# Performance work log

Measured on AMD Instinct MI355X. Metric: run time of the kernel, lower is better.

## Reference

```python
import jax, jax.numpy as jnp
import numpy as np

B, H, W, C = 8, 128, 128, 256
WS, SS, NH = 8, 4, 8          # window size, shift size, num heads
HD = C // NH                   # head dim = 32
N = WS * WS                    # tokens per window = 64
NW = (H // WS) * (W // WS)     # windows per image = 256


def _rel_pos_index():
    coords = np.stack(np.meshgrid(np.arange(WS), np.arange(WS), indexing='ij'))  # (2,WS,WS)
    cf = coords.reshape(2, -1)
    rc = (cf[:, :, None] - cf[:, None, :]).transpose(1, 2, 0)
    rc[:, :, 0] += WS - 1
    rc[:, :, 1] += WS - 1
    rc[:, :, 0] *= 2 * WS - 1
    return rc.sum(-1)  # (N, N) int


def _attn_mask():
    # shift mask for SW-MSA, built from static shapes (matches torch img_mask construction)
    img = np.zeros((1, H, W, 1))
    sl = (slice(0, -WS), slice(-WS, -SS), slice(-SS, None))
    cnt = 0
    for h in sl:
        for w in sl:
            img[:, h, w, :] = cnt
            cnt += 1
    mw = img.reshape(1, H // WS, WS, W // WS, WS, 1).transpose(0, 1, 3, 2, 4, 5).reshape(-1, N)
    am = mw[:, None, :] - mw[:, :, None]  # (NW, N, N)
    return np.where(am != 0, -100.0, 0.0).astype(np.float32)


RPI = jnp.asarray(_rel_pos_index())      # (N, N)
AMASK = jnp.asarray(_attn_mask())        # (NW, N, N)


def _ln(x, g, b):
    m = x.mean(-1, keepdims=True)
    v = x.var(-1, keepdims=True)
    return (x - m) / jnp.sqrt(v + 1e-5) * g + b


def setup_inputs() -> dict:
    key = jax.random.key(0)
    ks = jax.random.split(key, 8)
    s = lambda k, shp, sc: jax.random.normal(k, shp, jnp.float32) * sc
    return {
        'x': s(ks[0], (B, H * W, C), 1.0),
        'norm1_g': jnp.ones((C,), jnp.float32), 'norm1_b': jnp.zeros((C,), jnp.float32),
        'qkv_w': s(ks[1], (3 * C, C), 0.02), 'qkv_b': jnp.zeros((3 * C,), jnp.float32),
        'rpb_table': s(ks[2], ((2 * WS - 1) ** 2, NH), 0.02),
        'proj_w': s(ks[3], (C, C), 0.02), 'proj_b': jnp.zeros((C,), jnp.float32),
        'norm2_g': jnp.ones((C,), jnp.float32), 'norm2_b': jnp.zeros((C,), jnp.float32),
        'fc1_w': s(ks[4], (4 * C, C), 0.02), 'fc1_b': jnp.zeros((4 * C,), jnp.float32),
        'fc2_w': s(ks[5], (C, 4 * C), 0.02), 'fc2_b': jnp.zeros((C,), jnp.float32),
    }


def reference(x, norm1_g, norm1_b, qkv_w, qkv_b, rpb_table, proj_w, proj_b,
              norm2_g, norm2_b, fc1_w, fc1_b, fc2_w, fc2_b):
    shortcut = x
    h = _ln(x, norm1_g, norm1_b).reshape(B, H, W, C)
    # cyclic shift
    h = jnp.roll(h, (-SS, -SS), axis=(1, 2))
    # window partition -> (B*NW, N, C)
    xw = h.reshape(B, H // WS, WS, W // WS, WS, C).transpose(0, 1, 3, 2, 4, 5).reshape(-1, N, C)
    qkv = (xw @ qkv_w.T + qkv_b).reshape(-1, N, 3, NH, HD).transpose(2, 0, 3, 1, 4)
    q, k, v = qkv[0], qkv[1], qkv[2]           # (B*NW, NH, N, HD)
    attn = jnp.einsum('bhnd,bhmd->bhnm', q * (float(HD) ** -0.5), k)
    bias = rpb_table[RPI.reshape(-1)].reshape(N, N, NH).transpose(2, 0, 1)  # (NH, N, N)
    attn = attn + bias[None]
    attn = attn.reshape(B, NW, NH, N, N) + AMASK[None, :, None]
    attn = jax.nn.softmax(attn.reshape(-1, NH, N, N), axis=-1)
    xw = jnp.einsum('bhnm,bhmd->bnhd', attn, v).reshape(-1, N, C)
    xw = xw @ proj_w.T + proj_b
    # window reverse + reverse shift
    h = xw.reshape(B, H // WS, W // WS, WS, WS, C).transpose(0, 1, 3, 2, 4, 5).reshape(B, H, W, C)
    h = jnp.roll(h, (SS, SS), axis=(1, 2)).reshape(B, H * W, C)
    x = shortcut + h
    # MLP block
    m = _ln(x, norm2_g, norm2_b)
    m = jax.nn.gelu(m @ fc1_w.T + fc1_b, approximate=False) @ fc2_w.T + fc2_b
    return x + m
```

## Files before the change

kernel.cpp:

```cpp
#include <hip/hip_runtime.h>
#include <hip/hip_bf16.h>
#include <math.h>

#define B_   8
#define H_   128
#define W_   128
#define C_   256
#define WS_  8
#define SS_  4
#define NH_  8
#define HD_  32
#define MROWS 131072

typedef short bf16x8 __attribute__((ext_vector_type(8)));
typedef float f32x4  __attribute__((ext_vector_type(4)));

__device__ __forceinline__ unsigned short f2bf(float f) {
    unsigned int u = __float_as_uint(f);
    u += 0x7fffu + ((u >> 16) & 1u);
    return (unsigned short)(u >> 16);
}
__device__ __forceinline__ float bfl(unsigned int u) {
    return __uint_as_float(u << 16);
}
__device__ __forceinline__ float bfh(unsigned int u) {
    return __uint_as_float(u & 0xffff0000u);
}

__device__ __forceinline__ unsigned int pk2(float a, float b) {
    __hip_bfloat162 h = __float22bfloat162_rn(make_float2(a, b));
    unsigned int u;
    __builtin_memcpy(&u, &h, 4);
    return u;
}

__device__ __forceinline__ void gload16(const unsigned short* g, unsigned short* l) {
    __builtin_amdgcn_global_load_lds(
        (const __attribute__((address_space(1))) unsigned int*)(const void*)g,
        (__attribute__((address_space(3))) unsigned int*)(void*)l, 16, 0, 0);
}

__device__ __forceinline__ float fast_gelu2(float v) {
    return v * __builtin_amdgcn_rcpf(1.0f + __expf(-1.702f * v));
}

__global__ __launch_bounds__(256) void cvt4(const float* __restrict__ s,
                                            unsigned short* __restrict__ d, int n) {
    const int i = (blockIdx.x * 256 + threadIdx.x) * 4;
    if (i >= n) return;
    const float4 v = *(const float4*)(s + i);
    ushort4 o;
    o.x = f2bf(v.x); o.y = f2bf(v.y); o.z = f2bf(v.z); o.w = f2bf(v.w);
    *(ushort4*)(d + i) = o;
}

template<int SHIFT>
__global__ __launch_bounds__(256) void ln_kernel(const float* __restrict__ in,
                                                 const float* __restrict__ g,
                                                 const float* __restrict__ b,
                                                 unsigned short* __restrict__ out) {
    const int wid  = threadIdx.x >> 6;
    const int lane = threadIdx.x & 63;
    const int row  = blockIdx.x * 4 + wid;

    int src;
    if (SHIFT) {
        const int bimg = row >> 14;
        const int rem  = row & 16383;
        const int win  = rem >> 6;
        const int tok  = rem & 63;
        const int hp = (win >> 4) * 8 + (tok >> 3);
        const int wp = (win & 15) * 8 + (tok & 7);
        const int ho = (hp + SS_) & (H_ - 1);
        const int wo = (wp + SS_) & (W_ - 1);
        src = (bimg << 14) + ho * W_ + wo;
    } else {
        src = row;
    }

    const float4 v = ((const float4*)(in + (size_t)src * C_))[lane];
    float s  = v.x + v.y + v.z + v.w;
    float ss = v.x*v.x + v.y*v.y + v.z*v.z + v.w*v.w;
#pragma unroll
    for (int o = 1; o < 64; o <<= 1) {
        s  += __shfl_xor(s,  o, 64);
        ss += __shfl_xor(ss, o, 64);
    }
    const float mean = s * (1.0f / C_);
    const float var  = ss * (1.0f / C_) - mean * mean;
    const float rstd = rsqrtf(var + 1e-5f);

    const float4 gg = ((const float4*)g)[lane];
    const float4 bb = ((const float4*)b)[lane];
    ushort4 o4;
    o4.x = f2bf((v.x - mean) * rstd * gg.x + bb.x);
    o4.y = f2bf((v.y - mean) * rstd * gg.y + bb.y);
    o4.z = f2bf((v.z - mean) * rstd * gg.z + bb.z);
    o4.w = f2bf((v.w - mean) * rstd * gg.w + bb.w);
    *(ushort4*)(out + (size_t)row * C_ + lane * 4) = o4;
}

template<int N>
__global__ __launch_bounds__(256, 2) void gemm_nloop(const unsigned short* __restrict__ A,
                                                     const unsigned short* __restrict__ W,
                                                     const float* __restrict__ bias,
                                                     unsigned short* __restrict__ Cout) {
    __shared__ unsigned short W_lds[2][64 * 256];

    const int t    = threadIdx.x;
    const int wave = t >> 6, lane = t & 63;
    const int fr   = lane & 15, h = lane >> 4;
    const int m0   = blockIdx.x * 128;
    constexpr int NT = N / 64;

    bf16x8 aw[2][8];
    const unsigned short* Abase = A + (size_t)(m0 + wave * 32 + fr) * 256 + h * 8;
#pragma unroll
    for (int mi = 0; mi < 2; ++mi)
#pragma unroll
        for (int ks = 0; ks < 8; ++ks)
            aw[mi][ks] = *(const bf16x8*)(Abase + mi * 16 * 256 + ks * 32);

    auto stage = [&](int b, int nt) {
        const unsigned short* Wt = W + (size_t)nt * 64 * 256;
#pragma unroll
        for (int q = 0; q < 8; ++q) {
            const int d    = q * 4096 + t * 16;
            const int row  = d >> 9;
            const int colb = (d & 511) ^ ((row & 7) << 4);
            gload16(Wt + (size_t)row * 256 + (colb >> 1),
                    &W_lds[b][(q * 4096 + wave * 1024) >> 1]);
        }
    };

    stage(0, 0);
    __syncthreads();

    for (int nt = 0; nt < NT; ++nt) {
        if (nt + 1 < NT) stage((nt + 1) & 1, nt + 1);

        const char* buf = (const char*)W_lds[nt & 1];
        f32x4 acc[2][4] = {};
#pragma unroll
        for (int nj = 0; nj < 4; ++nj) {
            const int   wrow = nj * 16 + fr;
            const char* wb   = buf + wrow * 512;
            const int   swz  = (fr & 7) << 4;
            bf16x8 wf[8];
#pragma unroll
            for (int ks = 0; ks < 8; ++ks)
                wf[ks] = *(const bf16x8*)(wb + ((ks * 64 + h * 16) ^ swz));
#pragma unroll
            for (int ks = 0; ks < 8; ++ks) {
                acc[0][nj] = __builtin_amdgcn_mfma_f32_16x16x32_bf16(wf[ks], aw[0][ks], acc[0][nj], 0, 0, 0);
                acc[1][nj] = __builtin_amdgcn_mfma_f32_16x16x32_bf16(wf[ks], aw[1][ks], acc[1][nj], 0, 0, 0);
            }
        }

#pragma unroll
        for (int nj = 0; nj < 4; ++nj) {
            const int n = nt * 64 + nj * 16 + h * 4;
            const float4 bb = *(const float4*)&bias[n];
#pragma unroll
            for (int mi = 0; mi < 2; ++mi) {
                const int m = m0 + wave * 32 + mi * 16 + fr;
                uint2 pk;
                pk.x = pk2(acc[mi][nj][0] + bb.x, acc[mi][nj][1] + bb.y);
                pk.y = pk2(acc[mi][nj][2] + bb.z, acc[mi][nj][3] + bb.w);
                *(uint2*)&Cout[(size_t)m * N + n] = pk;
            }
        }
        __syncthreads();
    }
}

__global__ __launch_bounds__(512, 2) void mlp_fused(const unsigned short* __restrict__ A,
                                                    const unsigned short* __restrict__ W1,
                                                    const float* __restrict__ b1,
                                                    const unsigned short* __restrict__ W2,
                                                    const float* __restrict__ b2,
                                                    const unsigned short* __restrict__ x1b,
                                                    float* __restrict__ out) {
    __shared__ unsigned short W1_lds[2][32 * 256];
    __shared__ unsigned short W2_lds[2][256 * 32];
    __shared__ unsigned short G_lds [256 * 32];

    const int t    = threadIdx.x;
    const int wave = t >> 6, lane = t & 63;
    const int fr   = lane & 15, h = lane >> 4;
    const int wr   = wave >> 2, wc = wave & 3;
    const int m0   = blockIdx.x * 256;
    constexpr int NC = 32;

    bf16x8 aw[2][8];
    const unsigned short* Abase = A + (size_t)(m0 + wave * 32 + fr) * 256 + h * 8;
#pragma unroll
    for (int mi = 0; mi < 2; ++mi)
#pragma unroll
        for (int ks = 0; ks < 8; ++ks)
            aw[mi][ks] = *(const bf16x8*)(Abase + mi * 16 * 256 + ks * 32);

    auto stageW1 = [&](int b, int c) {
        const unsigned short* Wt = W1 + (size_t)c * 32 * 256;
#pragma unroll
        for (int q = 0; q < 2; ++q) {
            const int d    = q * 8192 + t * 16;
            const int row  = d >> 9;
            const int colb = (d & 511) ^ ((row & 7) << 4);
            gload16(Wt + (size_t)row * 256 + (colb >> 1),
                    &W1_lds[b][(q * 8192 + wave * 1024) >> 1]);
        }
    };
    auto stageW2 = [&](int b, int c) {
#pragma unroll
        for (int q = 0; q < 2; ++q) {
            const int d    = q * 8192 + t * 16;
            const int row  = d >> 6;
            const int colb = (d & 63) ^ ((row & 3) << 4);
            gload16(W2 + (size_t)row * 1024 + c * 32 + (colb >> 1),
                    &W2_lds[b][(q * 8192 + wave * 1024) >> 1]);
        }
    };

    auto fc1 = [&](int cc) {
        const char* buf = (const char*)W1_lds[cc & 1];
        const int   swz = (fr & 7) << 4;
#pragma unroll
        for (int nj = 0; nj < 2; ++nj) {
            const int   wrow = nj * 16 + fr;
            const char* wb   = buf + wrow * 512;
            bf16x8 wf[8];
#pragma unroll
            for (int ks = 0; ks < 8; ++ks)
                wf[ks] = *(const bf16x8*)(wb + ((ks * 64 + h * 16) ^ swz));
            f32x4 g0 = {}, g1 = {};
#pragma unroll
            for (int ks = 0; ks < 8; ++ks) {
                g0 = __builtin_amdgcn_mfma_f32_16x16x32_bf16(wf[ks], aw[0][ks], g0, 0, 0, 0);
                g1 = __builtin_amdgcn_mfma_f32_16x16x32_bf16(wf[ks], aw[1][ks], g1, 0, 0, 0);
            }
            const float4 bb = *(const float4*)&b1[cc * 32 + nj * 16 + h * 4];
            {
                const int row = wave * 32 + fr;
                const int off = (nj * 32 + h * 8) ^ ((row & 3) << 4);
                uint2 pk;
                pk.x = pk2(fast_gelu2(g0[0] + bb.x), fast_gelu2(g0[1] + bb.y));
                pk.y = pk2(fast_gelu2(g0[2] + bb.z), fast_gelu2(g0[3] + bb.w));
                *(uint2*)((char*)G_lds + row * 64 + off) = pk;
            }
            {
                const int row = wave * 32 + 16 + fr;
                const int off = (nj * 32 + h * 8) ^ ((row & 3) << 4);
                uint2 pk;
                pk.x = pk2(fast_gelu2(g1[0] + bb.x), fast_gelu2(g1[1] + bb.y));
                pk.y = pk2(fast_gelu2(g1[2] + bb.z), fast_gelu2(g1[3] + bb.w));
                *(uint2*)((char*)G_lds + row * 64 + off) = pk;
            }
        }
    };

    f32x4 acc2[8][4] = {};

    stageW1(0, 0);
    stageW2(0, 0);
    asm volatile("s_waitcnt vmcnt(0)" ::: "memory");
    __builtin_amdgcn_sched_barrier(0);
    __builtin_amdgcn_s_barrier();
    stageW1(1, 1);
    fc1(0);

    for (int c = 0; c < NC; ++c) {
        asm volatile("s_waitcnt vmcnt(0) lgkmcnt(0)" ::: "memory");
        __builtin_amdgcn_sched_barrier(0);
        __builtin_amdgcn_s_barrier();

        if (c + 2 < NC) stageW1(c & 1, c + 2);
        if (c + 1 < NC) stageW2((c + 1) & 1, c + 1);

        {
            const char* Gb = (const char*)G_lds;
            const char* Wb = (const char*)W2_lds[c & 1];
            bf16x8 gf[8];
#pragma unroll
            for (int mi2 = 0; mi2 < 8; ++mi2) {
                const int grow = wr * 128 + mi2 * 16 + fr;
                gf[mi2] = *(const bf16x8*)(Gb + grow * 64 + ((h * 16) ^ ((grow & 3) << 4)));
            }
#pragma unroll
            for (int nj2 = 0; nj2 < 4; ++nj2) {
                const int wrow2 = wc * 64 + nj2 * 16 + fr;
                const bf16x8 w2f = *(const bf16x8*)(Wb + wrow2 * 64 + ((h * 16) ^ ((wrow2 & 3) << 4)));
#pragma unroll
                for (int mi2 = 0; mi2 < 8; ++mi2)
                    acc2[mi2][nj2] = __builtin_amdgcn_mfma_f32_16x16x32_bf16(
                        w2f, gf[mi2], acc2[mi2][nj2], 0, 0, 0);
            }
        }

        __builtin_amdgcn_s_barrier();

        if (c + 1 < NC) fc1(c + 1);
    }

    float4 bv[4];
#pragma unroll
    for (int nj2 = 0; nj2 < 4; ++nj2)
        bv[nj2] = *(const float4*)&b2[wc * 64 + nj2 * 16 + h * 4];

#pragma unroll
    for (int mi2 = 0; mi2 < 8; ++mi2) {
        const int m = m0 + wr * 128 + mi2 * 16 + fr;
#pragma unroll
        for (int nj2 = 0; nj2 < 4; ++nj2) {
            const int n = wc * 64 + nj2 * 16 + h * 4;
            const size_t idx = (size_t)m * 256 + n;
            const uint2 rb = *(const uint2*)&x1b[idx];
            float4 o;
            o.x = acc2[mi2][nj2][0] + bv[nj2].x + bfl(rb.x);
            o.y = acc2[mi2][nj2][1] + bv[nj2].y + bfh(rb.x);
            o.z = acc2[mi2][nj2][2] + bv[nj2].z + bfl(rb.y);
            o.w = acc2[mi2][nj2][3] + bv[nj2].w + bfh(rb.y);
            *(float4*)&out[idx] = o;
        }
    }
}

__global__ __launch_bounds__(256, 2) void proj_ln2(const unsigned short* __restrict__ A,
                                                   const unsigned short* __restrict__ W,
                                                   const float* __restrict__ bias,
                                                   const float* __restrict__ resid,
                                                   const float* __restrict__ g2,
                                                   const float* __restrict__ b2,
                                                   unsigned short* __restrict__ x1b,
                                                   unsigned short* __restrict__ ln2out) {
    __shared__ unsigned short W_lds[2][64 * 256];

    const int t    = threadIdx.x;
    const int wave = t >> 6, lane = t & 63;
    const int fr   = lane & 15, h = lane >> 4;
    const int m0   = blockIdx.x * 128;

    bf16x8 aw[2][8];
    const unsigned short* Abase = A + (size_t)(m0 + wave * 32 + fr) * 256 + h * 8;
#pragma unroll
    for (int mi = 0; mi < 2; ++mi)
#pragma unroll
        for (int ks = 0; ks < 8; ++ks)
            aw[mi][ks] = *(const bf16x8*)(Abase + mi * 16 * 256 + ks * 32);

    auto stage = [&](int b, int nt) {
        const unsigned short* Wt = W + (size_t)nt * 64 * 256;
#pragma unroll
        for (int q = 0; q < 8; ++q) {
            const int d    = q * 4096 + t * 16;
            const int row  = d >> 9;
            const int colb = (d & 511) ^ ((row & 7) << 4);
            gload16(Wt + (size_t)row * 256 + (colb >> 1),
                    &W_lds[b][(q * 4096 + wave * 1024) >> 1]);
        }
    };

    stage(0, 0);
    __syncthreads();

    f32x4 acc[2][16] = {};
    for (int nt = 0; nt < 4; ++nt) {
        if (nt < 3) stage((nt + 1) & 1, nt + 1);
        const char* buf = (const char*)W_lds[nt & 1];
#pragma unroll
        for (int nj = 0; nj < 4; ++nj) {
            const int   wrow = nj * 16 + fr;
            const char* wb   = buf + wrow * 512;
            const int   swz  = (fr & 7) << 4;
            bf16x8 wf[8];
#pragma unroll
            for (int ks = 0; ks < 8; ++ks)
                wf[ks] = *(const bf16x8*)(wb + ((ks * 64 + h * 16) ^ swz));
            switch (nt) {
            case 0:
#pragma unroll
                for (int ks = 0; ks < 8; ++ks) {
                    acc[0][0 + nj] = __builtin_amdgcn_mfma_f32_16x16x32_bf16(wf[ks], aw[0][ks], acc[0][0 + nj], 0, 0, 0);
                    acc[1][0 + nj] = __builtin_amdgcn_mfma_f32_16x16x32_bf16(wf[ks], aw[1][ks], acc[1][0 + nj], 0, 0, 0);
                } break;
            case 1:
#pragma unroll
                for (int ks = 0; ks < 8; ++ks) {
                    acc[0][4 + nj] = __builtin_amdgcn_mfma_f32_16x16x32_bf16(wf[ks], aw[0][ks], acc[0][4 + nj], 0, 0, 0);
                    acc[1][4 + nj] = __builtin_amdgcn_mfma_f32_16x16x32_bf16(wf[ks], aw[1][ks], acc[1][4 + nj], 0, 0, 0);
                } break;
            case 2:
#pragma unroll
                for (int ks = 0; ks < 8; ++ks) {
                    acc[0][8 + nj] = __builtin_amdgcn_mfma_f32_16x16x32_bf16(wf[ks], aw[0][ks], acc[0][8 + nj], 0, 0, 0);
                    acc[1][8 + nj] = __builtin_amdgcn_mfma_f32_16x16x32_bf16(wf[ks], aw[1][ks], acc[1][8 + nj], 0, 0, 0);
                } break;
            default:
#pragma unroll
                for (int ks = 0; ks < 8; ++ks) {
                    acc[0][12 + nj] = __builtin_amdgcn_mfma_f32_16x16x32_bf16(wf[ks], aw[0][ks], acc[0][12 + nj], 0, 0, 0);
                    acc[1][12 + nj] = __builtin_amdgcn_mfma_f32_16x16x32_bf16(wf[ks], aw[1][ks], acc[1][12 + nj], 0, 0, 0);
                } break;
            }
        }
        __syncthreads();
    }

#pragma unroll
    for (int mi = 0; mi < 2; ++mi) {
        const int m    = m0 + wave * 32 + mi * 16 + fr;
        const int bimg = m >> 14;
        const int rem  = m & 16383;
        const int win  = rem >> 6;
        const int tok  = rem & 63;
        const int hp = (win >> 4) * 8 + (tok >> 3);
        const int wp = (win & 15) * 8 + (tok & 7);
        const int ho = (hp + SS_) & (H_ - 1);
        const int wo = (wp + SS_) & (W_ - 1);
        const size_t drow = ((size_t)(bimg << 14) + ho * W_ + wo) * 256;

        float sum = 0.0f, ssum = 0.0f;
#pragma unroll
        for (int u = 0; u < 16; ++u) {
            const int n = (u >> 2) * 64 + (u & 3) * 16 + h * 4;
            const float4 bb = *(const float4*)&bias[n];
            const float4 r4 = *(const float4*)&resid[drow + n];
            float4 v;
            v.x = acc[mi][u][0] + bb.x + r4.x;
            v.y = acc[mi][u][1] + bb.y + r4.y;
            v.z = acc[mi][u][2] + bb.z + r4.z;
            v.w = acc[mi][u][3] + bb.w + r4.w;
            uint2 pk;
            pk.x = pk2(v.x, v.y);
            pk.y = pk2(v.z, v.w);
            *(uint2*)&x1b[drow + n] = pk;
            sum  += v.x + v.y + v.z + v.w;
            ssum += v.x*v.x + v.y*v.y + v.z*v.z + v.w*v.w;
        }
        sum  += __shfl_xor(sum, 16, 64);  sum  += __shfl_xor(sum, 32, 64);
        ssum += __shfl_xor(ssum, 16, 64); ssum += __shfl_xor(ssum, 32, 64);
        const float mean = sum * (1.0f / 256.0f);
        const float rstd = rsqrtf(ssum * (1.0f / 256.0f) - mean * mean + 1e-5f);

#pragma unroll
        for (int u = 0; u < 16; ++u) {
            const int n = (u >> 2) * 64 + (u & 3) * 16 + h * 4;
            const uint2 rb = *(const uint2*)&x1b[drow + n];
            const float4 gg = *(const float4*)&g2[n];
            const float4 bb = *(const float4*)&b2[n];
            uint2 pk;
            pk.x = pk2((bfl(rb.x) - mean) * rstd * gg.x + bb.x,
                       (bfh(rb.x) - mean) * rstd * gg.y + bb.y);
            pk.y = pk2((bfl(rb.y) - mean) * rstd * gg.z + bb.z,
                       (bfh(rb.y) - mean) * rstd * gg.w + bb.w);
            *(uint2*)&ln2out[drow + n] = pk;
        }
    }
}

__device__ __forceinline__ int grp_(int p) { return p < (H_ - WS_) ? 0 : (p < (H_ - SS_) ? 1 : 2); }

__global__ __launch_bounds__(256) void attn_kernel(const unsigned short* __restrict__ qkv,
                                                   const float* __restrict__ rpb,
                                                   unsigned short* __restrict__ out) {
    __shared__ unsigned short P [4][64 * 72];
    __shared__ unsigned short Vt[4][32 * 72];
    __shared__ float rpb_s[232];

    const int t    = threadIdx.x;
    const int wid  = t >> 6, lane = t & 63;
    const int head = blockIdx.x & 7;
    const int win  = (blockIdx.x >> 3) * 4 + wid;
    const int fr   = lane & 15, h = lane >> 4;

    if (t < 225) rpb_s[t] = rpb[t * 8 + head];
    __syncthreads();

    const size_t qbase = (size_t)win * 64 * 768 + head * HD_;

    bf16x8 ak[4], bq[4];
#pragma unroll
    for (int ki = 0; ki < 4; ++ki)
        ak[ki] = *(const bf16x8*)&qkv[qbase + (size_t)(ki * 16 + fr) * 768 + 256 + h * 8];
#pragma unroll
    for (int qj = 0; qj < 4; ++qj)
        bq[qj] = *(const bf16x8*)&qkv[qbase + (size_t)(qj * 16 + fr) * 768 + h * 8];

    {
        const unsigned short* vrow = &qkv[qbase + (size_t)lane * 768 + 512];
#pragma unroll
        for (int dv = 0; dv < 32; dv += 8) {
            bf16x8 v8 = *(const bf16x8*)&vrow[dv];
#pragma unroll
            for (int j = 0; j < 8; ++j)
                Vt[wid][(dv + j) * 72 + lane] = ((unsigned short*)&v8)[j];
        }
    }

    f32x4 st[4][4] = {};
#pragma unroll
    for (int ki = 0; ki < 4; ++ki)
#pragma unroll
        for (int qj = 0; qj < 4; ++qj)
            st[ki][qj] = __builtin_amdgcn_mfma_f32_16x16x32_bf16(ak[ki], bq[qj], st[ki][qj], 0, 0, 0);

    const int wim = win & 255;
    const int whb = (wim >> 4) * 8, wwb = (wim & 15) * 8;
    const float qscale = 0.17677669529663687f;

#pragma unroll
    for (int qj = 0; qj < 4; ++qj) {
        const int q  = qj * 16 + fr;
        const int yq = q >> 3, xq = q & 7;
        const int gq = grp_(whb + yq) * 3 + grp_(wwb + xq);
        float s[16];
#pragma unroll
        for (int ki = 0; ki < 4; ++ki)
#pragma unroll
            for (int r = 0; r < 4; ++r) {
                const int k  = ki * 16 + h * 4 + r;
                const int yk = k >> 3, xk = k & 7;
                const int gk = grp_(whb + yk) * 3 + grp_(wwb + xk);
                float v = fmaf(st[ki][qj][r], qscale,
                               rpb_s[(yq - yk + 7) * 15 + (xq - xk + 7)]);
                if (gk != gq) v -= 100.0f;
                s[ki * 4 + r] = v;
            }
        float m = s[0];
#pragma unroll
        for (int i = 1; i < 16; ++i) m = fmaxf(m, s[i]);
        m = fmaxf(m, __shfl_xor(m, 16, 64));
        m = fmaxf(m, __shfl_xor(m, 32, 64));
        float sum = 0.0f;
#pragma unroll
        for (int i = 0; i < 16; ++i) { s[i] = __expf(s[i] - m); sum += s[i]; }
        sum += __shfl_xor(sum, 16, 64);
        sum += __shfl_xor(sum, 32, 64);
        const float rinv = __builtin_amdgcn_rcpf(sum);
#pragma unroll
        for (int ki = 0; ki < 4; ++ki)
#pragma unroll
            for (int rp = 0; rp < 4; rp += 2) {
                const unsigned int lo = f2bf(s[ki * 4 + rp]     * rinv);
                const unsigned int hi = f2bf(s[ki * 4 + rp + 1] * rinv);
                *(unsigned int*)&P[wid][q * 72 + ki * 16 + h * 4 + rp] = lo | (hi << 16);
            }
    }

    f32x4 oacc[4][2] = {};
#pragma unroll
    for (int ks = 0; ks < 2; ++ks) {
        bf16x8 pa[4], vb[2];
#pragma unroll
        for (int qi = 0; qi < 4; ++qi)
            pa[qi] = *(const bf16x8*)&P[wid][(qi * 16 + fr) * 72 + ks * 32 + h * 8];
#pragma unroll
        for (int nj = 0; nj < 2; ++nj)
            vb[nj] = *(const bf16x8*)&Vt[wid][(nj * 16 + fr) * 72 + ks * 32 + h * 8];
#pragma unroll
        for (int qi = 0; qi < 4; ++qi)
#pragma unroll
            for (int nj = 0; nj < 2; ++nj)
                oacc[qi][nj] = __builtin_amdgcn_mfma_f32_16x16x32_bf16(pa[qi], vb[nj], oacc[qi][nj], 0, 0, 0);
    }

#pragma unroll
    for (int qi = 0; qi < 4; ++qi)
#pragma unroll
        for (int nj = 0; nj < 2; ++nj)
#pragma unroll
            for (int r = 0; r < 4; ++r) {
                const int q = qi * 16 + h * 4 + r;
                const int d = nj * 16 + fr;
                out[((size_t)win * 64 + q) * C_ + head * HD_ + d] = f2bf(oacc[qi][nj][r]);
            }
}

extern "C" void kernel_launch(void* const* d_in, const int* in_sizes, int n_in,
                              void* d_out, int out_size, void* d_ws, size_t ws_size,
                              hipStream_t stream) {
    const float* x      = (const float*)d_in[0];
    const float* n1g    = (const float*)d_in[1];
    const float* n1b    = (const float*)d_in[2];
    const float* qkv_w  = (const float*)d_in[3];
    const float* qkv_b  = (const float*)d_in[4];
    const float* rpb    = (const float*)d_in[5];
    const float* proj_w = (const float*)d_in[6];
    const float* proj_b = (const float*)d_in[7];
    const float* n2g    = (const float*)d_in[8];
    const float* n2b    = (const float*)d_in[9];
    const float* fc1_w  = (const float*)d_in[10];
    const float* fc1_b  = (const float*)d_in[11];
    const float* fc2_w  = (const float*)d_in[12];
    const float* fc2_b  = (const float*)d_in[13];
    float* out = (float*)d_out;

    unsigned short* wq  = (unsigned short*)d_ws;
    unsigned short* rA  = wq + (1u << 20);
    unsigned short* rB  = rA + 33554432u;
    unsigned short* rB2 = rB + 100663296u;
    unsigned short* x1b = rB;

    unsigned short* qkv_wb  = wq;
    unsigned short* proj_wb = wq + 196608;
    unsigned short* fc1_wb  = wq + 262144;
    unsigned short* fc2_wb  = wq + 524288;

    cvt4<<<192, 256, 0, stream>>>(qkv_w,  qkv_wb,  196608);
    cvt4<<<64,  256, 0, stream>>>(proj_w, proj_wb, 65536);
    cvt4<<<256, 256, 0, stream>>>(fc1_w,  fc1_wb,  262144);
    cvt4<<<256, 256, 0, stream>>>(fc2_w,  fc2_wb,  262144);

    ln_kernel<1><<<MROWS / 4, 256, 0, stream>>>(x, n1g, n1b, rA);
    gemm_nloop<768><<<MROWS / 128, 256, 0, stream>>>(rA, qkv_wb, qkv_b, rB);
    attn_kernel<<<(2048 / 4) * NH_, 256, 0, stream>>>(rB, rpb, rB2);
    proj_ln2<<<MROWS / 128, 256, 0, stream>>>(rB2, proj_wb, proj_b, x, n2g, n2b, x1b, rA);
    mlp_fused<<<MROWS / 256, 512, 0, stream>>>(rA, fc1_wb, fc1_b, fc2_wb, fc2_b, x1b, out);
}
```

Before: 582.3 us.

## Fuse LN1 with shifted window gather into QKV GEMM; single-buffer W2 in MLP

LayerNorm1, including the cyclic shift and window gather, now runs inside the QKV GEMM prologue. Each wave normalizes its rows in registers and packs them straight into bf16 MFMA fragments, so the bf16 LN output no longer goes to HBM and is not read back, and one launch is dropped. Separately, the MLP kernel keeps a single W2 LDS buffer, loaded after the barrier instead of double-buffered ahead, and raises its launch_bounds occupancy hint from 2 to 4. This cuts LDS use so more blocks can be resident, but W2 load latency is less hidden and register pressure is higher.

```diff
diff --git a/kernel.cpp b/kernel.cpp
--- a/kernel.cpp
+++ b/kernel.cpp
@@ -54,86 +54,84 @@
     *(ushort4*)(d + i) = o;
 }
 
-template<int SHIFT>
-__global__ __launch_bounds__(256) void ln_kernel(const float* __restrict__ in,
-                                                 const float* __restrict__ g,
-                                                 const float* __restrict__ b,
-                                                 unsigned short* __restrict__ out) {
-    const int wid  = threadIdx.x >> 6;
-    const int lane = threadIdx.x & 63;
-    const int row  = blockIdx.x * 4 + wid;
-
-    int src;
-    if (SHIFT) {
-        const int bimg = row >> 14;
-        const int rem  = row & 16383;
+template<int N>
+__global__ __launch_bounds__(256, 2) void ln1_qkv(const float* __restrict__ x,
+                                                  const float* __restrict__ g1,
+                                                  const float* __restrict__ b1n,
+                                                  const unsigned short* __restrict__ W,
+                                                  const float* __restrict__ bias,
+                                                  unsigned short* __restrict__ Cout) {
+    __shared__ unsigned short W_lds[2][64 * 256];
+
+    const int t    = threadIdx.x;
+    const int wave = t >> 6, lane = t & 63;
+    const int fr   = lane & 15, h = lane >> 4;
+    const int m0   = blockIdx.x * 128;
+    constexpr int NT = N / 64;
+
+    auto stage = [&](int b, int nt) {
+        const unsigned short* Wt = W + (size_t)nt * 64 * 256;
+#pragma unroll
+        for (int q = 0; q < 8; ++q) {
+            const int d    = q * 4096 + t * 16;
+            const int row  = d >> 9;
+            const int colb = (d & 511) ^ ((row & 7) << 4);
+            gload16(Wt + (size_t)row * 256 + (colb >> 1),
+                    &W_lds[b][(q * 4096 + wave * 1024) >> 1]);
+        }
+    };
+
+    stage(0, 0);
+
+    bf16x8 aw[2][8];
+#pragma unroll
+    for (int mi = 0; mi < 2; ++mi) {
+        const int m    = m0 + wave * 32 + mi * 16 + fr;
+        const int bimg = m >> 14;
+        const int rem  = m & 16383;
         const int win  = rem >> 6;
         const int tok  = rem & 63;
         const int hp = (win >> 4) * 8 + (tok >> 3);
         const int wp = (win & 15) * 8 + (tok & 7);
         const int ho = (hp + SS_) & (H_ - 1);
         const int wo = (wp + SS_) & (W_ - 1);
-        src = (bimg << 14) + ho * W_ + wo;
-    } else {
-        src = row;
-    }
-
-    const float4 v = ((const float4*)(in + (size_t)src * C_))[lane];
-    float s  = v.x + v.y + v.z + v.w;
-    float ss = v.x*v.x + v.y*v.y + v.z*v.z + v.w*v.w;
-#pragma unroll
-    for (int o = 1; o < 64; o <<= 1) {
-        s  += __shfl_xor(s,  o, 64);
-        ss += __shfl_xor(ss, o, 64);
-    }
-    const float mean = s * (1.0f / C_);
-    const float var  = ss * (1.0f / C_) - mean * mean;
-    const float rstd = rsqrtf(var + 1e-5f);
-
-    const float4 gg = ((const float4*)g)[lane];
-    const float4 bb = ((const float4*)b)[lane];
-    ushort4 o4;
-    o4.x = f2bf((v.x - mean) * rstd * gg.x + bb.x);
-    o4.y = f2bf((v.y - mean) * rstd * gg.y + bb.y);
-    o4.z = f2bf((v.z - mean) * rstd * gg.z + bb.z);
-    o4.w = f2bf((v.w - mean) * rstd * gg.w + bb.w);
-    *(ushort4*)(out + (size_t)row * C_ + lane * 4) = o4;
-}
-
-template<int N>
-__global__ __launch_bounds__(256, 2) void gemm_nloop(const unsigned short* __restrict__ A,
-                                                     const unsigned short* __restrict__ W,
-                                                     const float* __restrict__ bias,
-                                                     unsigned short* __restrict__ Cout) {
-    __shared__ unsigned short W_lds[2][64 * 256];
-
-    const int t    = threadIdx.x;
-    const int wave = t >> 6, lane = t & 63;
-    const int fr   = lane & 15, h = lane >> 4;
-    const int m0   = blockIdx.x * 128;
-    constexpr int NT = N / 64;
-
-    bf16x8 aw[2][8];
-    const unsigned short* Abase = A + (size_t)(m0 + wave * 32 + fr) * 256 + h * 8;
-#pragma unroll
-    for (int mi = 0; mi < 2; ++mi)
-#pragma unroll
-        for (int ks = 0; ks < 8; ++ks)
-            aw[mi][ks] = *(const bf16x8*)(Abase + mi * 16 * 256 + ks * 32);
-
-    auto stage = [&](int b, int nt) {
-        const unsigned short* Wt = W + (size_t)nt * 64 * 256;
-#pragma unroll
-        for (int q = 0; q < 8; ++q) {
-            const int d    = q * 4096 + t * 16;
-            const int row  = d >> 9;
-            const int colb = (d & 511) ^ ((row & 7) << 4);
-            gload16(Wt + (size_t)row * 256 + (colb >> 1),
-                    &W_lds[b][(q * 4096 + wave * 1024) >> 1]);
-        }
-    };
-
-    stage(0, 0);
+        const float* xr = x + ((size_t)(bimg << 14) + ho * W_ + wo) * C_;
+
+        float4 va[8], vb[8];
+        float s = 0.0f, ss = 0.0f;
+#pragma unroll
+        for (int ks = 0; ks < 8; ++ks) {
+            va[ks] = *(const float4*)&xr[ks * 32 + h * 8];
+            vb[ks] = *(const float4*)&xr[ks * 32 + h * 8 + 4];
+            s  += va[ks].x + va[ks].y + va[ks].z + va[ks].w
+                + vb[ks].x + vb[ks].y + vb[ks].z + vb[ks].w;
+            ss += va[ks].x*va[ks].x + va[ks].y*va[ks].y + va[ks].z*va[ks].z + va[ks].w*va[ks].w
+                + vb[ks].x*vb[ks].x + vb[ks].y*vb[ks].y + vb[ks].z*vb[ks].z + vb[ks].w*vb[ks].w;
+        }
+        s  += __shfl_xor(s, 16, 64);  s  += __shfl_xor(s, 32, 64);
+        ss += __shfl_xor(ss, 16, 64); ss += __shfl_xor(ss, 32, 64);
+        const float mean = s * (1.0f / 256.0f);
+        const float rstd = rsqrtf(ss * (1.0f / 256.0f) - mean * mean + 1e-5f);
+
+#pragma unroll
+        for (int ks = 0; ks < 8; ++ks) {
+            const float4 g0 = *(const float4*)&g1 [ks * 32 + h * 8];
+            const float4 g4 = *(const float4*)&g1 [ks * 32 + h * 8 + 4];
+            const float4 c0 = *(const float4*)&b1n[ks * 32 + h * 8];
+            const float4 c4 = *(const float4*)&b1n[ks * 32 + h * 8 + 4];
+            uint4 u;
+            u.x = pk2((va[ks].x - mean) * rstd * g0.x + c0.x,
+                      (va[ks].y - mean) * rstd * g0.y + c0.y);
+            u.y = pk2((va[ks].z - mean) * rstd * g0.z + c0.z,
+                      (va[ks].w - mean) * rstd * g0.w + c0.w);
+            u.z = pk2((vb[ks].x - mean) * rstd * g4.x + c4.x,
+                      (vb[ks].y - mean) * rstd * g4.y + c4.y);
+            u.w = pk2((vb[ks].z - mean) * rstd * g4.z + c4.z,
+                      (vb[ks].w - mean) * rstd * g4.w + c4.w);
+            aw[mi][ks] = *(bf16x8*)&u;
+        }
+    }
+
     __syncthreads();
 
     for (int nt = 0; nt < NT; ++nt) {
@@ -174,7 +172,7 @@
     }
 }
 
-__global__ __launch_bounds__(512, 2) void mlp_fused(const unsigned short* __restrict__ A,
+__global__ __launch_bounds__(512, 4) void mlp_fused(const unsigned short* __restrict__ A,
                                                     const unsigned short* __restrict__ W1,
                                                     const float* __restrict__ b1,
                                                     const unsigned short* __restrict__ W2,
@@ -182,7 +180,7 @@
                                                     const unsigned short* __restrict__ x1b,
                                                     float* __restrict__ out) {
     __shared__ unsigned short W1_lds[2][32 * 256];
-    __shared__ unsigned short W2_lds[2][256 * 32];
+    __shared__ unsigned short W2_lds[256 * 32];
     __shared__ unsigned short G_lds [256 * 32];
 
     const int t    = threadIdx.x;
@@ -211,14 +209,14 @@
                     &W1_lds[b][(q * 8192 + wave * 1024) >> 1]);
         }
     };
-    auto stageW2 = [&](int b, int c) {
+    auto stageW2 = [&](int c) {
 #pragma unroll
         for (int q = 0; q < 2; ++q) {
             const int d    = q * 8192 + t * 16;
             const int row  = d >> 6;
             const int colb = (d & 63) ^ ((row & 3) << 4);
             gload16(W2 + (size_t)row * 1024 + c * 32 + (colb >> 1),
-                    &W2_lds[b][(q * 8192 + wave * 1024) >> 1]);
+                    &W2_lds[(q * 8192 + wave * 1024) >> 1]);
         }
     };
 
@@ -262,7 +260,7 @@
     f32x4 acc2[8][4] = {};
 
     stageW1(0, 0);
-    stageW2(0, 0);
+    stageW2(0);
     asm volatile("s_waitcnt vmcnt(0)" ::: "memory");
     __builtin_amdgcn_sched_barrier(0);
     __builtin_amdgcn_s_barrier();
@@ -275,11 +273,10 @@
         __builtin_amdgcn_s_barrier();
 
         if (c + 2 < NC) stageW1(c & 1, c + 2);
-        if (c + 1 < NC) stageW2((c + 1) & 1, c + 1);
 
         {
             const char* Gb = (const char*)G_lds;
-            const char* Wb = (const char*)W2_lds[c & 1];
+            const char* Wb = (const char*)W2_lds;
             bf16x8 gf[8];
 #pragma unroll
             for (int mi2 = 0; mi2 < 8; ++mi2) {
@@ -299,7 +296,10 @@
 
         __builtin_amdgcn_s_barrier();
 
-        if (c + 1 < NC) fc1(c + 1);
+        if (c + 1 < NC) {
+            stageW2(c + 1);
+            fc1(c + 1);
+        }
     }
 
     float4 bv[4];
@@ -611,8 +611,7 @@
     cvt4<<<256, 256, 0, stream>>>(fc1_w,  fc1_wb,  262144);
     cvt4<<<256, 256, 0, stream>>>(fc2_w,  fc2_wb,  262144);
 
-    ln_kernel<1><<<MROWS / 4, 256, 0, stream>>>(x, n1g, n1b, rA);
-    gemm_nloop<768><<<MROWS / 128, 256, 0, stream>>>(rA, qkv_wb, qkv_b, rB);
+    ln1_qkv<768><<<MROWS / 128, 256, 0, stream>>>(x, n1g, n1b, qkv_wb, qkv_b, rB);
     attn_kernel<<<(2048 / 4) * NH_, 256, 0, stream>>>(rB, rpb, rB2);
     proj_ln2<<<MROWS / 128, 256, 0, stream>>>(rB2, proj_wb, proj_b, x, n2g, n2b, x1b, rA);
     mlp_fused<<<MROWS / 256, 512, 0, stream>>>(rA, fc1_wb, fc1_b, fc2_wb, fc2_b, x1b, out);
```

Result: slower. 1.338 ms (+129.8%).
